# Optimization experiments

Hardware: AMD Instinct MI355X
Metric: run time of the kernel (lower is better)

## Reference

```python
import jax, jax.numpy as jnp
import numpy as np

NUM_SAMPLES = 4_194_304  # 2**22 samples (~87s @ 48kHz) -> memory-bound streaming IIR


def setup_inputs() -> dict:
    key = jax.random.key(0)
    k1, k2 = jax.random.split(key)
    # [attack, decay, filter_lp, filter_hp, gain]; uniform(0,1) is in the valid clamped range
    parameters = jax.random.uniform(k1, (5,), dtype=jnp.float32)
    noise = jax.random.normal(k2, (NUM_SAMPLES,), dtype=jnp.float32)
    return {"parameters": parameters, "noise": noise}


def _one_pole_lowpass(x, c):
    # y[n] = (1 - c) * x[n] + c * y[n-1]
    def step(y_prev, xn):
        y = (1.0 - c) * xn + c * y_prev
        return y, y
    _, y = jax.lax.scan(step, jnp.zeros((), x.dtype), x)
    return y


def _one_pole_highpass(x, c):
    # y[n] = c * (y[n-1] + x[n] - x[n-1])
    dx = jnp.concatenate([x[:1], x[1:] - x[:-1]])
    def step(y_prev, d):
        y = c * (y_prev + d)
        return y, y
    _, y = jax.lax.scan(step, jnp.zeros((), x.dtype), dx)
    return y


def reference(parameters, noise):
    attack = jnp.clip(parameters[0], 1e-7, None)
    decay = jnp.clip(parameters[1], 1e-7, None)
    filter_lp = jnp.clip(parameters[2], 1e-7, 0.99)
    filter_hp = jnp.clip(parameters[3], 1e-7, 0.99)
    gain = jnp.clip(parameters[4], 1e-7, None)

    n = noise.shape[0]
    t = jnp.linspace(0.0, 1.0, n, dtype=noise.dtype)  # matches registered 'time' buffer
    # exponential attack/decay envelope
    envelope = (1.0 - jnp.exp(-t / attack)) * jnp.exp(-t / decay)

    filtered = _one_pole_lowpass(noise, filter_lp)
    filtered = _one_pole_highpass(filtered, filter_hp)
    return filtered * envelope * gain
```

## Files before the change

### kernel.cpp

```cpp
#include <hip/hip_runtime.h>
#include <math.h>


#define BLOCK 128
#define CHUNK 64
#define SAMP  (BLOCK * CHUNK)
#define WMAX  1600
#define TWORDS (SAMP + WMAX)
#define LDSW  (TWORDS + TWORDS / 32)

__device__ __forceinline__ int pidx(int i) { return i + (i >> 5); }

__global__ __launch_bounds__(BLOCK) void noisegen_kernel(
    const float* __restrict__ params,
    const float* __restrict__ noise,
    float* __restrict__ out, int n)
{
    __shared__ float lds[LDSW];

    float attack = fmaxf(params[0], 1e-7f);
    float decay  = fmaxf(params[1], 1e-7f);
    float c_lp   = fminf(fmaxf(params[2], 1e-7f), 0.99f);
    float c_hp   = fminf(fmaxf(params[3], 1e-7f), 0.99f);
    float gain   = fmaxf(params[4], 1e-7f);

    float cmax = fmaxf(c_lp, c_hp);
    int W = (int)ceilf(-16.12f / logf(cmax));
    W = min(max(W, 4), WMAX);
    int H = (W + 31) & ~31;

    int tid = threadIdx.x;
    int B = blockIdx.x * SAMP;
    int base = B - H;
    int T = H + SAMP;

    for (int v = tid; v < (T >> 2); v += BLOCK) {
        int i = v << 2;
        int g = base + i;
        float4 val = make_float4(0.f, 0.f, 0.f, 0.f);
        if (g >= 0 && g + 3 < n) {
            val = *(const float4*)(noise + g);
        }
        int p = pidx(i);
        lds[p] = val.x; lds[p + 1] = val.y; lds[p + 2] = val.z; lds[p + 3] = val.w;
    }
    __syncthreads();

    float omc = 1.0f - c_lp;
    float y = 0.f, yprev = 0.f, z = 0.f;
    int l0 = H + tid * CHUNK;

    for (int j = l0 - W; j < l0; ++j) {
        float x = lds[pidx(j)];
        y = fmaf(c_lp, y, omc * x);
        z = c_hp * (z + (y - yprev));
        yprev = y;
    }
    __syncthreads();

    float inv_nm1 = 1.0f / (float)(n - 1);
    float ia = -1.0f / attack;
    float id = -1.0f / decay;
    int g0 = B + tid * CHUNK;

    #pragma unroll 4
    for (int j = 0; j < CHUNK; ++j) {
        int gi = g0 + j;
        if (gi >= n) break;
        int p = pidx(l0 + j);
        float x = lds[p];
        y = fmaf(c_lp, y, omc * x);
        z = c_hp * (z + (y - yprev));
        yprev = y;
        float t = (float)gi * inv_nm1;
        float env = (1.0f - __expf(t * ia)) * __expf(t * id);
        lds[p] = z * env * gain;
    }
    __syncthreads();

    for (int v = tid; v < (SAMP >> 2); v += BLOCK) {
        int i = v << 2;
        int g = B + i;
        if (g + 3 < n) {
            int p = pidx(H + i);
            *(float4*)(out + g) = make_float4(lds[p], lds[p + 1], lds[p + 2], lds[p + 3]);
        }
    }
}

extern "C" void kernel_launch(void* const* d_in, const int* in_sizes, int n_in,
                              void* d_out, int out_size, void* d_ws, size_t ws_size,
                              hipStream_t stream) {
    const float* params = (const float*)d_in[0];
    const float* noise  = (const float*)d_in[1];
    float* out = (float*)d_out;
    int n = in_sizes[1];
    int grid = (n + SAMP - 1) / SAMP;
    noisegen_kernel<<<grid, BLOCK, 0, stream>>>(params, noise, out, n);
}
```

Measured before the change: 83.49 us.

## Replace per-thread warmup with block-wide affine scan of filter state

Each block now loads a fixed halo plus its tile and runs a local filter pass per thread. It then combines the chunk end states with a log-step Hillis-Steele scan over the composed lowpass/highpass transition matrices, so each thread starts its output chunk from the exact carried state instead of a parameter-dependent warmup window. The per-sample exp calls for the envelope become a running multiplicative recurrence, and the padded LDS indexing is dropped in favour of an odd chunk stride. In exchange it adds 8 synchronised scan steps, a fixed 1280-sample halo that is read and filtered redundantly, and possible rounding drift in the envelope.

```diff
diff --git a/kernel.cpp b/kernel.cpp
--- a/kernel.cpp
+++ b/kernel.cpp
@@ -2,88 +2,125 @@
 #include <math.h>
 
 
-#define BLOCK 128
-#define CHUNK 64
-#define SAMP  (BLOCK * CHUNK)
-#define WMAX  1600
-#define TWORDS (SAMP + WMAX)
-#define LDSW  (TWORDS + TWORDS / 32)
-
-__device__ __forceinline__ int pidx(int i) { return i + (i >> 5); }
+#define BLOCK 256
+#define CHUNK 37
+#define TWORDS (BLOCK * CHUNK)
+#define SAMP   8192
+#define HALO   (TWORDS - SAMP)
 
 __global__ __launch_bounds__(BLOCK) void noisegen_kernel(
     const float* __restrict__ params,
     const float* __restrict__ noise,
     float* __restrict__ out, int n)
 {
-    __shared__ float lds[LDSW];
+    __shared__ __align__(16) float xs[TWORDS];
+    __shared__ float sy[2][BLOCK];
+    __shared__ float sz[2][BLOCK];
 
     float attack = fmaxf(params[0], 1e-7f);
     float decay  = fmaxf(params[1], 1e-7f);
-    float c_lp   = fminf(fmaxf(params[2], 1e-7f), 0.99f);
-    float c_hp   = fminf(fmaxf(params[3], 1e-7f), 0.99f);
+    float a      = fminf(fmaxf(params[2], 1e-7f), 0.99f);
+    float b      = fminf(fmaxf(params[3], 1e-7f), 0.99f);
     float gain   = fmaxf(params[4], 1e-7f);
+    float omc    = 1.0f - a;
 
-    float cmax = fmaxf(c_lp, c_hp);
-    int W = (int)ceilf(-16.12f / logf(cmax));
-    W = min(max(W, 4), WMAX);
-    int H = (W + 31) & ~31;
+    int tid  = threadIdx.x;
+    int B    = blockIdx.x * SAMP;
+    int base = B - HALO;
 
-    int tid = threadIdx.x;
-    int B = blockIdx.x * SAMP;
-    int base = B - H;
-    int T = H + SAMP;
-
-    for (int v = tid; v < (T >> 2); v += BLOCK) {
+    for (int v = tid; v < (TWORDS >> 2); v += BLOCK) {
         int i = v << 2;
         int g = base + i;
-        float4 val = make_float4(0.f, 0.f, 0.f, 0.f);
-        if (g >= 0 && g + 3 < n) {
+        float4 val;
+        if (g >= 0 && g + 4 <= n) {
             val = *(const float4*)(noise + g);
+        } else {
+            val.x = (g     >= 0 && g     < n) ? noise[g]     : 0.0f;
+            val.y = (g + 1 >= 0 && g + 1 < n) ? noise[g + 1] : 0.0f;
+            val.z = (g + 2 >= 0 && g + 2 < n) ? noise[g + 2] : 0.0f;
+            val.w = (g + 3 >= 0 && g + 3 < n) ? noise[g + 3] : 0.0f;
         }
-        int p = pidx(i);
-        lds[p] = val.x; lds[p + 1] = val.y; lds[p + 2] = val.z; lds[p + 3] = val.w;
+        *(float4*)(xs + i) = val;
     }
     __syncthreads();
 
-    float omc = 1.0f - c_lp;
-    float y = 0.f, yprev = 0.f, z = 0.f;
-    int l0 = H + tid * CHUNK;
+    int l0 = tid * CHUNK;
+    float yv = 0.0f, zv = 0.0f;
+    #pragma unroll 4
+    for (int j = 0; j < CHUNK; ++j) {
+        float x  = xs[l0 + j];
+        float yn = fmaf(a, yv, omc * x);
+        zv = b * (zv + (yn - yv));
+        yv = yn;
+    }
+    sy[0][tid] = yv;
+    sz[0][tid] = zv;
+    __syncthreads();
 
-    for (int j = l0 - W; j < l0; ++j) {
-        float x = lds[pidx(j)];
-        y = fmaf(c_lp, y, omc * x);
-        z = c_hp * (z + (y - yprev));
-        yprev = y;
+    float ma = a, mw = b * (a - 1.0f), mb = b;
+    float pa = ma, pw = mw, pb = mb;
+    { float qa=pa*pa, qw=pw*pa+pb*pw, qb=pb*pb; pa=qa; pw=qw; pb=qb; }
+    float p4a, p4w, p4b;
+    { p4a=pa*pa; p4w=pw*pa+pb*pw; p4b=pb*pb; }
+    float ta=p4a, tw=p4w, tb=p4b;
+    { float qa=ta*ta, qw=tw*ta+tb*tw, qb=tb*tb; ta=qa; tw=qw; tb=qb; }
+    { float qa=ta*ta, qw=tw*ta+tb*tw, qb=tb*tb; ta=qa; tw=qw; tb=qb; }
+    { float qa=ta*ta, qw=tw*ta+tb*tw, qb=tb*tb; ta=qa; tw=qw; tb=qb; }
+    { float qa=ta*p4a, qw=tw*p4a+tb*p4w, qb=tb*p4b; ta=qa; tw=qw; tb=qb; }
+    { float qa=ta*ma,  qw=tw*ma +tb*mw,  qb=tb*mb;  pa=qa; pw=qw; pb=qb; }
+
+    int cur = 0;
+    for (int d = 1; d < BLOCK; d <<= 1) {
+        float ny = sy[cur][tid], nz = sz[cur][tid];
+        if (tid >= d) {
+            float py = sy[cur][tid - d], pz = sz[cur][tid - d];
+            ny = fmaf(pa, py, ny);
+            nz = fmaf(pw, py, fmaf(pb, pz, nz));
+        }
+        sy[1 - cur][tid] = ny;
+        sz[1 - cur][tid] = nz;
+        cur = 1 - cur;
+        float qa = pa * pa, qw = pw * pa + pb * pw, qb = pb * pb;
+        pa = qa; pw = qw; pb = qb;
+        __syncthreads();
     }
-    __syncthreads();
+
+    float y0 = 0.0f, z0 = 0.0f;
+    if (tid > 0) { y0 = sy[cur][tid - 1]; z0 = sz[cur][tid - 1]; }
 
     float inv_nm1 = 1.0f / (float)(n - 1);
     float ia = -1.0f / attack;
     float id = -1.0f / decay;
-    int g0 = B + tid * CHUNK;
+    float t0 = (float)(base + l0) * inv_nm1;
+    float ea = __expf(ia * t0);
+    float ed = __expf(id * t0);
+    float ra = __expf(ia * inv_nm1);
+    float rd = __expf(id * inv_nm1);
 
+    yv = y0; zv = z0;
     #pragma unroll 4
     for (int j = 0; j < CHUNK; ++j) {
-        int gi = g0 + j;
-        if (gi >= n) break;
-        int p = pidx(l0 + j);
-        float x = lds[p];
-        y = fmaf(c_lp, y, omc * x);
-        z = c_hp * (z + (y - yprev));
-        yprev = y;
-        float t = (float)gi * inv_nm1;
-        float env = (1.0f - __expf(t * ia)) * __expf(t * id);
-        lds[p] = z * env * gain;
+        int li = l0 + j;
+        float x  = xs[li];
+        float yn = fmaf(a, yv, omc * x);
+        zv = b * (zv + (yn - yv));
+        yv = yn;
+        if (li >= HALO) {
+            float env = (1.0f - ea) * ed;
+            xs[li] = zv * env * gain;
+        }
+        ea *= ra; ed *= rd;
     }
     __syncthreads();
 
     for (int v = tid; v < (SAMP >> 2); v += BLOCK) {
         int i = v << 2;
         int g = B + i;
-        if (g + 3 < n) {
-            int p = pidx(H + i);
-            *(float4*)(out + g) = make_float4(lds[p], lds[p + 1], lds[p + 2], lds[p + 3]);
+        if (g + 4 <= n) {
+            *(float4*)(out + g) = *(const float4*)(xs + HALO + i);
+        } else {
+            for (int c = 0; c < 4; ++c)
+                if (g + c < n) out[g + c] = xs[HALO + i + c];
         }
     }
 }
```

Result: faster. 78.14 us (-6.4%).
